# Kernel tuning notes

Measured on AMD Instinct MI355X. Metric: run time of the kernel, lower is better.

The kernel has to match this reference:

```python
import jax, jax.numpy as jnp
import numpy as np

B, N, H, D, FE = 4, 1024, 64, 64, 16  # batch, nodes, hidden_in, out_dim, edge_feat


def setup_inputs() -> dict:
    key = jax.random.key(0)
    k0, k1, k2, k3 = jax.random.split(key, 4)
    h0 = jax.random.normal(k0, (B, N, H), dtype=jnp.float32)
    e = jax.random.normal(k1, (B, N, N, FE), dtype=jnp.float32)
    # fc: Linear(H -> D, bias=False), xavier-normal-ish scale
    w_fc = jax.random.normal(k2, (D, H), dtype=jnp.float32) * (2.0 / np.sqrt(H + D))
    # attn_fc: Linear(2*D + FE -> 1, bias=False), stored as a flat vector
    w_attn = jax.random.normal(k3, (2 * D + FE,), dtype=jnp.float32) * (2.0 / np.sqrt(2 * D + FE + 1))
    return {"h0": h0, "e": e, "w_fc": w_fc, "w_attn": w_attn}


def reference(h0, e, w_fc, w_attn):
    # z = fc(h0): [B, N, D]
    z = jnp.einsum('bnh,dh->bnd', h0, w_fc)
    d = z.shape[-1]
    # attn_fc on concat(z1, z2, m): z1[i*N+j] = z[j], z2[i*N+j] = z[i], m[i*N+j] = e[i, j]
    a1, a2, a3 = w_attn[:d], w_attn[d:2 * d], w_attn[2 * d:]
    sj = jnp.einsum('bnd,d->bn', z, a1)            # score part from z1 (source j)
    si = jnp.einsum('bnd,d->bn', z, a2)            # score part from z2 (target i)
    se = jnp.einsum('bijf,f->bij', e, a3)          # edge score part
    # scores s[b, i, j], then leaky_relu (slope 0.01 as in torch default)
    s = jax.nn.leaky_relu(si[:, :, None] + sj[:, None, :] + se)
    # softmax over the flattened N*N pair axis (dim=1 of [B, N*N, 1] in torch)
    b = s.shape[0]
    alpha = jax.nn.softmax(s.reshape(b, -1), axis=1).reshape(s.shape)  # [B, N, N]
    # h_t[b, i] = sum_j alpha[b, i, j] * z_expanded[b, i, j], where z_expanded[b, i, j] = z[b, i]
    h_t = jnp.sum(alpha, axis=2)[:, :, None] * z
    return h_t
```

## Files before the change

### kernel.cpp

```cpp
#include <hip/hip_runtime.h>
#include <hip/hip_bf16.h>

#define NTOK   1024
#define NROWS  4096
#define HD     64

__global__ __launch_bounds__(64) void k1_fc(
    const float* __restrict__ h0, const float* __restrict__ w_fc,
    const float* __restrict__ w_attn,
    float* __restrict__ z, float* __restrict__ si, float* __restrict__ sj)
{
    const int row = blockIdx.x;
    const int d   = threadIdx.x;
    __shared__ float sh[HD];
    sh[d] = h0[row * HD + d];
    __syncthreads();

    float acc = 0.f;
    #pragma unroll
    for (int h = 0; h < HD; ++h)
        acc = fmaf(sh[h], w_fc[d * HD + h], acc);
    z[row * HD + d] = acc;

    float v1 = acc * w_attn[d];
    float v2 = acc * w_attn[HD + d];
    #pragma unroll
    for (int off = 32; off; off >>= 1) {
        v1 += __shfl_down(v1, off);
        v2 += __shfl_down(v2, off);
    }
    if (d == 0) { sj[row] = v1; si[row] = v2; }
}

__global__ __launch_bounds__(256) void k2_row(
    const float* __restrict__ e, const float* __restrict__ w_attn,
    const float* __restrict__ si, const float* __restrict__ sj,
    float* __restrict__ Mrow, float* __restrict__ Rrow)
{
    const int row = blockIdx.x;
    const int b   = row >> 10;
    const int tid = threadIdx.x;

    const float4* a3v = (const float4*)(w_attn + 2 * HD);
    const float4 a30 = a3v[0], a31 = a3v[1], a32 = a3v[2], a33 = a3v[3];

    const float  si_r = si[row];
    const float4* ev  = (const float4*)(e + (size_t)row * (NTOK * 16));
    const float* sjb  = sj + b * NTOK;

    float sv[4];
    #pragma unroll
    for (int it = 0; it < 4; ++it) {
        const int j = tid + it * 256;
        const float4* p = ev + (size_t)j * 4;
        const float4 e0 = p[0], e1 = p[1], e2 = p[2], e3 = p[3];
        float se = e0.x*a30.x + e0.y*a30.y + e0.z*a30.z + e0.w*a30.w;
        se      += e1.x*a31.x + e1.y*a31.y + e1.z*a31.z + e1.w*a31.w;
        se      += e2.x*a32.x + e2.y*a32.y + e2.z*a32.z + e2.w*a32.w;
        se      += e3.x*a33.x + e3.y*a33.y + e3.z*a33.z + e3.w*a33.w;
        float s = si_r + sjb[j] + se;
        s = (s > 0.f) ? s : 0.01f * s;
        sv[it] = s;
    }

    float m = fmaxf(fmaxf(sv[0], sv[1]), fmaxf(sv[2], sv[3]));
    float r = __expf(sv[0] - m) + __expf(sv[1] - m)
            + __expf(sv[2] - m) + __expf(sv[3] - m);

    #pragma unroll
    for (int off = 1; off < 64; off <<= 1) {
        float om  = __shfl_xor(m, off);
        float orr = __shfl_xor(r, off);
        float nm  = fmaxf(m, om);
        r = r * __expf(m - nm) + orr * __expf(om - nm);
        m = nm;
    }

    __shared__ float sm[4], sr[4];
    if ((tid & 63) == 0) { sm[tid >> 6] = m; sr[tid >> 6] = r; }
    __syncthreads();
    if (tid == 0) {
        float M = sm[0], R = sr[0];
        #pragma unroll
        for (int w = 1; w < 4; ++w) {
            float om = sm[w], orr = sr[w];
            float nm = fmaxf(M, om);
            R = R * __expf(M - nm) + orr * __expf(om - nm);
            M = nm;
        }
        Mrow[row] = M; Rrow[row] = R;
    }
}

__global__ __launch_bounds__(1024) void k3_batch(
    const float* __restrict__ Mrow, const float* __restrict__ Rrow,
    float* __restrict__ mz)
{
    const int b = blockIdx.x;
    const int i = threadIdx.x;
    const float Mi = Mrow[b * NTOK + i];
    const float Ri = Rrow[b * NTOK + i];

    __shared__ float red[16];
    __shared__ float bc;

    float m = Mi;
    #pragma unroll
    for (int off = 32; off; off >>= 1) m = fmaxf(m, __shfl_xor(m, off));
    if ((i & 63) == 0) red[i >> 6] = m;
    __syncthreads();
    if (i == 0) {
        float mm = red[0];
        #pragma unroll
        for (int w = 1; w < 16; ++w) mm = fmaxf(mm, red[w]);
        bc = mm;
    }
    __syncthreads();
    const float mb = bc;

    float ssum = Ri * __expf(Mi - mb);
    #pragma unroll
    for (int off = 32; off; off >>= 1) ssum += __shfl_xor(ssum, off);
    __syncthreads();
    if ((i & 63) == 0) red[i >> 6] = ssum;
    __syncthreads();
    if (i == 0) {
        float Z = 0.f;
        #pragma unroll
        for (int w = 0; w < 16; ++w) Z += red[w];
        mz[b * 2]     = mb;
        mz[b * 2 + 1] = Z;
    }
}

__global__ __launch_bounds__(256) void k4_out(
    const float* __restrict__ z, const float* __restrict__ Mrow,
    const float* __restrict__ Rrow, const float* __restrict__ mz,
    float* __restrict__ out)
{
    const int idx = blockIdx.x * 256 + threadIdx.x;
    const int row = idx >> 4;
    const int b   = row >> 10;
    const float scale = Rrow[row] * __expf(Mrow[row] - mz[b * 2]) / mz[b * 2 + 1];
    const float4 zv = ((const float4*)z)[idx];
    float4 o;
    o.x = zv.x * scale; o.y = zv.y * scale;
    o.z = zv.z * scale; o.w = zv.w * scale;
    ((float4*)out)[idx] = o;
}

extern "C" void kernel_launch(void* const* d_in, const int* in_sizes, int n_in,
                              void* d_out, int out_size, void* d_ws, size_t ws_size,
                              hipStream_t stream)
{
    const float* h0     = (const float*)d_in[0];
    const float* e      = (const float*)d_in[1];
    const float* w_fc   = (const float*)d_in[2];
    const float* w_attn = (const float*)d_in[3];
    float* out = (float*)d_out;

    float* ws   = (float*)d_ws;
    float* z    = ws;
    float* si   = z  + NROWS * HD;
    float* sj   = si + NROWS;
    float* Mrow = sj + NROWS;
    float* Rrow = Mrow + NROWS;
    float* mz   = Rrow + NROWS;

    k1_fc   <<<NROWS, 64,   0, stream>>>(h0, w_fc, w_attn, z, si, sj);
    k2_row  <<<NROWS, 256,  0, stream>>>(e, w_attn, si, sj, Mrow, Rrow);
    k3_batch<<<4,     1024, 0, stream>>>(Mrow, Rrow, mz);
    k4_out  <<<256,   256,  0, stream>>>(z, Mrow, Rrow, mz, out);
}
```

Before: 371.9 us.

## Coalesce edge-feature loads in row kernel and tile FC kernel over 16 rows

The row-softmax kernel now has each thread load one consecutive float4 of the edge tensor, so a wavefront reads contiguous memory. Four lanes combine their partial dot products with shuffles. Every lane in a quad then carries the same score, so the exp-sum is four times too large and is scaled by 0.25. The FC kernel now processes 16 rows per block with w_fc staged in padded shared memory, which cuts block count and redundant weight loads.

```diff
diff --git a/kernel.cpp b/kernel.cpp
--- a/kernel.cpp
+++ b/kernel.cpp
@@ -5,31 +5,44 @@
 #define NROWS  4096
 #define HD     64
 
-__global__ __launch_bounds__(64) void k1_fc(
+__global__ __launch_bounds__(256) void k1_fc(
     const float* __restrict__ h0, const float* __restrict__ w_fc,
     const float* __restrict__ w_attn,
     float* __restrict__ z, float* __restrict__ si, float* __restrict__ sj)
 {
-    const int row = blockIdx.x;
-    const int d   = threadIdx.x;
-    __shared__ float sh[HD];
-    sh[d] = h0[row * HD + d];
+    __shared__ float wfs[HD * 65];
+    __shared__ float h0s[16 * HD];
+
+    const int tid = threadIdx.x;
+    for (int k = tid; k < HD * HD; k += 256) {
+        int d = k >> 6, h = k & 63;
+        wfs[d * 65 + h] = w_fc[k];
+    }
+    const int row0 = blockIdx.x * 16;
+    for (int k = tid; k < 16 * HD; k += 256)
+        h0s[k] = h0[row0 * HD + k];
     __syncthreads();
 
-    float acc = 0.f;
-    #pragma unroll
-    for (int h = 0; h < HD; ++h)
-        acc = fmaf(sh[h], w_fc[d * HD + h], acc);
-    z[row * HD + d] = acc;
+    const int lane = tid & 63, wave = tid >> 6;
+    const float a1 = w_attn[lane];
+    const float a2 = w_attn[HD + lane];
 
-    float v1 = acc * w_attn[d];
-    float v2 = acc * w_attn[HD + d];
-    #pragma unroll
-    for (int off = 32; off; off >>= 1) {
-        v1 += __shfl_down(v1, off);
-        v2 += __shfl_down(v2, off);
+    for (int rr = wave; rr < 16; rr += 4) {
+        float acc = 0.f;
+        #pragma unroll
+        for (int h = 0; h < HD; ++h)
+            acc = fmaf(h0s[rr * HD + h], wfs[lane * 65 + h], acc);
+        const int row = row0 + rr;
+        z[row * HD + lane] = acc;
+
+        float v1 = acc * a1, v2 = acc * a2;
+        #pragma unroll
+        for (int off = 32; off; off >>= 1) {
+            v1 += __shfl_xor(v1, off);
+            v2 += __shfl_xor(v2, off);
+        }
+        if (lane == 0) { sj[row] = v1; si[row] = v2; }
     }
-    if (d == 0) { sj[row] = v1; si[row] = v2; }
 }
 
 __global__ __launch_bounds__(256) void k2_row(
@@ -42,30 +55,32 @@
     const int tid = threadIdx.x;
 
     const float4* a3v = (const float4*)(w_attn + 2 * HD);
-    const float4 a30 = a3v[0], a31 = a3v[1], a32 = a3v[2], a33 = a3v[3];
+    const float4  a3q = a3v[tid & 3];
 
-    const float  si_r = si[row];
-    const float4* ev  = (const float4*)(e + (size_t)row * (NTOK * 16));
-    const float* sjb  = sj + b * NTOK;
+    const float   si_r = si[row];
+    const float4* ev   = (const float4*)(e + (size_t)row * (NTOK * 16));
+    const float*  sjb  = sj + b * NTOK;
 
-    float sv[4];
+    float sv[16];
     #pragma unroll
-    for (int it = 0; it < 4; ++it) {
-        const int j = tid + it * 256;
-        const float4* p = ev + (size_t)j * 4;
-        const float4 e0 = p[0], e1 = p[1], e2 = p[2], e3 = p[3];
-        float se = e0.x*a30.x + e0.y*a30.y + e0.z*a30.z + e0.w*a30.w;
-        se      += e1.x*a31.x + e1.y*a31.y + e1.z*a31.z + e1.w*a31.w;
-        se      += e2.x*a32.x + e2.y*a32.y + e2.z*a32.z + e2.w*a32.w;
-        se      += e3.x*a33.x + e3.y*a33.y + e3.z*a33.z + e3.w*a33.w;
-        float s = si_r + sjb[j] + se;
+    for (int it = 0; it < 16; ++it) {
+        const int c = it * 256 + tid;
+        const float4 ec = ev[c];
+        float p = ec.x * a3q.x + ec.y * a3q.y + ec.z * a3q.z + ec.w * a3q.w;
+        p += __shfl_xor(p, 1);
+        p += __shfl_xor(p, 2);
+        const int j = it * 64 + (tid >> 2);
+        float s = si_r + sjb[j] + p;
         s = (s > 0.f) ? s : 0.01f * s;
         sv[it] = s;
     }
 
-    float m = fmaxf(fmaxf(sv[0], sv[1]), fmaxf(sv[2], sv[3]));
-    float r = __expf(sv[0] - m) + __expf(sv[1] - m)
-            + __expf(sv[2] - m) + __expf(sv[3] - m);
+    float m = sv[0];
+    #pragma unroll
+    for (int it = 1; it < 16; ++it) m = fmaxf(m, sv[it]);
+    float r = 0.f;
+    #pragma unroll
+    for (int it = 0; it < 16; ++it) r += __expf(sv[it] - m);
 
     #pragma unroll
     for (int off = 1; off < 64; off <<= 1) {
@@ -88,7 +103,8 @@
             R = R * __expf(M - nm) + orr * __expf(om - nm);
             M = nm;
         }
-        Mrow[row] = M; Rrow[row] = R;
+        Mrow[row] = M;
+        Rrow[row] = R * 0.25f;
     }
 }
 
@@ -167,7 +183,7 @@
     float* Rrow = Mrow + NROWS;
     float* mz   = Rrow + NROWS;
 
-    k1_fc   <<<NROWS, 64,   0, stream>>>(h0, w_fc, w_attn, z, si, sj);
+    k1_fc   <<<256,   256,  0, stream>>>(h0, w_fc, w_attn, z, si, sj);
     k2_row  <<<NROWS, 256,  0, stream>>>(e, w_attn, si, sj, Mrow, Rrow);
     k3_batch<<<4,     1024, 0, stream>>>(Mrow, Rrow, mz);
     k4_out  <<<256,   256,  0, stream>>>(z, Mrow, Rrow, mz, out);
```

New measurement: 373.8 us. Within noise of the previous version (+0.5%).
